# Optimization experiments

Hardware: AMD Instinct MI355X
Metric: run time of the kernel (lower is better)

Reference implementation:

```python
import jax, jax.numpy as jnp
import numpy as np

D_MODEL = 1024
NUM_HEADS = 16
D_K = D_MODEL // NUM_HEADS
B, S = 4, 2048


def setup_inputs() -> dict:
    key = jax.random.key(0)
    ks = jax.random.split(key, 11)
    s = 1.0 / np.sqrt(D_MODEL)  # torch Linear default init scale (uniform bound)
    def lin(k):
        kw, kb = jax.random.split(k)
        W = jax.random.uniform(kw, (D_MODEL, D_MODEL), jnp.float32, -s, s)
        b = jax.random.uniform(kb, (D_MODEL,), jnp.float32, -s, s)
        return W, b
    Wq, bq = lin(ks[0])
    Wk, bk = lin(ks[1])
    Wv, bv = lin(ks[2])
    Wo, bo = lin(ks[3])
    query = jax.random.normal(ks[4], (B, S, D_MODEL), jnp.float32)
    key_t = jax.random.normal(ks[5], (B, S, D_MODEL), jnp.float32)
    value = jax.random.normal(ks[6], (B, S, D_MODEL), jnp.float32)
    mask = jnp.ones((B, 1, 1, S), jnp.int32)
    return {"query": query, "key": key_t, "value": value, "mask": mask,
            "Wq": Wq, "bq": bq, "Wk": Wk, "bk": bk, "Wv": Wv, "bv": bv,
            "Wo": Wo, "bo": bo}


def _split_heads(x):
    # (B, S, D) -> (B, H, S, d_k)
    b, s, _ = x.shape
    return x.reshape(b, s, NUM_HEADS, D_K).transpose(0, 2, 1, 3)


def _mha(query, key, value, mask, Wq, bq, Wk, bk, Wv, bv, Wo, bo):
    Q = _split_heads(query @ Wq.T + bq)
    K = _split_heads(key @ Wk.T + bk)
    V = _split_heads(value @ Wv.T + bv)
    scores = jnp.einsum('bhqd,bhkd->bhqk', Q, K) / np.sqrt(D_K)
    scores = jnp.where(mask == 0, jnp.float32(-1e9), scores)
    attn = jax.nn.softmax(scores, axis=-1)
    out = jnp.einsum('bhqk,bhkd->bhqd', attn, V)  # (B,H,S,d_k)
    out = out.transpose(0, 2, 1, 3).reshape(out.shape[0], out.shape[2], D_MODEL)
    return out @ Wo.T + bo


def reference(query, key, value, mask, Wq, bq, Wk, bk, Wv, bv, Wo, bo):
    return _mha(query, key, value, mask, Wq, bq, Wk, bk, Wv, bv, Wo, bo)
```

## Files before the change

kernel.cpp:

```cpp
#include <hip/hip_runtime.h>


typedef unsigned short u16;
typedef __attribute__((ext_vector_type(8))) short short8;
typedef __attribute__((ext_vector_type(4))) float f32x4;

__device__ __forceinline__ u16 f2bf(float f) {
  union { float f; unsigned int u; } v; v.f = f;
  return (u16)((v.u + 0x7FFFu + ((v.u >> 16) & 1u)) >> 16);
}

__device__ __forceinline__ void gll16(const void* gptr, void* lptr) {
  __builtin_amdgcn_global_load_lds(
      (const __attribute__((address_space(1))) unsigned int*)gptr,
      (__attribute__((address_space(3))) unsigned int*)lptr, 16, 0, 0);
}

__global__ void cvt_x(const float* __restrict__ s, u16* __restrict__ d, int n) {
  const int i = (blockIdx.x * 256 + threadIdx.x) * 8;
  if (i >= n) return;
  f32x4 a = *(const f32x4*)(s + i);
  f32x4 b = *(const f32x4*)(s + i + 4);
  short8 r;
  r[0] = (short)f2bf(a[0]); r[1] = (short)f2bf(a[1]);
  r[2] = (short)f2bf(a[2]); r[3] = (short)f2bf(a[3]);
  r[4] = (short)f2bf(b[0]); r[5] = (short)f2bf(b[1]);
  r[6] = (short)f2bf(b[2]); r[7] = (short)f2bf(b[3]);
  *(short8*)(d + i) = r;
}

__global__ void cvt_x3(const float* __restrict__ q, const float* __restrict__ k,
                       const float* __restrict__ v, u16* __restrict__ d) {
  const int z = blockIdx.y;
  const float* s = (z == 0) ? q : (z == 1) ? k : v;
  const int i = (blockIdx.x * 256 + threadIdx.x) * 8;
  u16* dz = d + (size_t)z * 8388608;
  f32x4 a = *(const f32x4*)(s + i);
  f32x4 b = *(const f32x4*)(s + i + 4);
  short8 r;
  r[0] = (short)f2bf(a[0]); r[1] = (short)f2bf(a[1]);
  r[2] = (short)f2bf(a[2]); r[3] = (short)f2bf(a[3]);
  r[4] = (short)f2bf(b[0]); r[5] = (short)f2bf(b[1]);
  r[6] = (short)f2bf(b[2]); r[7] = (short)f2bf(b[3]);
  *(short8*)(dz + i) = r;
}

__global__ void cvt_w4(const float* __restrict__ w0, const float* __restrict__ w1,
                       const float* __restrict__ w2, const float* __restrict__ w3,
                       u16* __restrict__ d) {
  const int z = blockIdx.y;
  const float* s = (z == 0) ? w0 : (z == 1) ? w1 : (z == 2) ? w2 : w3;
  const int i = (blockIdx.x * 256 + threadIdx.x) * 8;
  u16* dz = d + (size_t)z * 1048576;
  f32x4 a = *(const f32x4*)(s + i);
  f32x4 b = *(const f32x4*)(s + i + 4);
  short8 r;
  r[0] = (short)f2bf(a[0]); r[1] = (short)f2bf(a[1]);
  r[2] = (short)f2bf(a[2]); r[3] = (short)f2bf(a[3]);
  r[4] = (short)f2bf(b[0]); r[5] = (short)f2bf(b[1]);
  r[6] = (short)f2bf(b[2]); r[7] = (short)f2bf(b[3]);
  *(short8*)(dz + i) = r;
}

#define GM 128
#define GN 128
#define GK 32

template <typename TC, bool TRANS>
__global__ __launch_bounds__(256, 3) void gemm_bb(
    const u16* __restrict__ A, const u16* __restrict__ W,
    const float* __restrict__ bias, TC* __restrict__ C,
    int M, int N, int K, float scale)
{
  __shared__ __align__(16) u16 As[2][GM * GK];
  __shared__ __align__(16) u16 Bs[2][GN * GK];

  const int tid  = threadIdx.x;
  const int lane = tid & 63;
  const int l15  = lane & 15;
  const int quad = lane >> 4;
  const int wave = tid >> 6;
  const int bm = blockIdx.y * GM;
  const int bn = blockIdx.x * GN;
  const int wm = (wave >> 1) * 64;
  const int wn = (wave & 1) * 64;

  const f32x4 zero4 = {0.f, 0.f, 0.f, 0.f};
  f32x4 acc[4][4];
#pragma unroll
  for (int i = 0; i < 4; i++)
#pragma unroll
    for (int j = 0; j < 4; j++) acc[i][j] = zero4;

  const int srow = tid >> 2;
  const int chl  = (tid & 3) ^ ((tid >> 3) & 3);
  const u16* Ag = A + (size_t)(bm + srow) * K + chl * 8;
  const u16* Wg = W + (size_t)(bn + srow) * K + chl * 8;
  const size_t rowskip = (size_t)64 * K;
  const int chpA = quad ^ ((l15 >> 1) & 3);

  gll16(Ag, &As[0][tid * 8]);
  gll16(Ag + rowskip, &As[0][tid * 8 + 2048]);
  gll16(Wg, &Bs[0][tid * 8]);
  gll16(Wg + rowskip, &Bs[0][tid * 8 + 2048]);

  int buf = 0;
  for (int k0 = 0; k0 < K; k0 += GK) {
    __syncthreads();
    if (k0 + GK < K) {
      const int nb = buf ^ 1;
      gll16(Ag + k0 + GK, &As[nb][tid * 8]);
      gll16(Ag + k0 + GK + rowskip, &As[nb][tid * 8 + 2048]);
      gll16(Wg + k0 + GK, &Bs[nb][tid * 8]);
      gll16(Wg + k0 + GK + rowskip, &Bs[nb][tid * 8 + 2048]);
    }

    short8 af[4], bfr[4];
#pragma unroll
    for (int mi = 0; mi < 4; mi++)
      af[mi] = *(const short8*)&As[buf][(wm + mi * 16 + l15) * GK + chpA * 8];
#pragma unroll
    for (int ni = 0; ni < 4; ni++)
      bfr[ni] = *(const short8*)&Bs[buf][(wn + ni * 16 + l15) * GK + chpA * 8];
#pragma unroll
    for (int mi = 0; mi < 4; mi++)
#pragma unroll
      for (int ni = 0; ni < 4; ni++)
        acc[mi][ni] = __builtin_amdgcn_mfma_f32_16x16x32_bf16(
            af[mi], bfr[ni], acc[mi][ni], 0, 0, 0);
    buf ^= 1;
  }

  float bval[4];
#pragma unroll
  for (int ni = 0; ni < 4; ni++) bval[ni] = bias[bn + wn + ni * 16 + l15];
#pragma unroll
  for (int mi = 0; mi < 4; mi++) {
    const int m0 = bm + wm + mi * 16 + quad * 4;
#pragma unroll
    for (int ni = 0; ni < 4; ni++) {
      const int n = bn + wn + ni * 16 + l15;
      if constexpr (TRANS) {
        ushort4 w;
        w.x = f2bf((acc[mi][ni][0] + bval[ni]) * scale);
        w.y = f2bf((acc[mi][ni][1] + bval[ni]) * scale);
        w.z = f2bf((acc[mi][ni][2] + bval[ni]) * scale);
        w.w = f2bf((acc[mi][ni][3] + bval[ni]) * scale);
        *(ushort4*)((u16*)C + (size_t)n * M + m0) = w;
      } else {
#pragma unroll
        for (int r = 0; r < 4; r++) {
          const float v = (acc[mi][ni][r] + bval[ni]) * scale;
          if constexpr (sizeof(TC) == 2)
            C[(size_t)(m0 + r) * N + n] = f2bf(v);
          else
            C[(size_t)(m0 + r) * N + n] = v;
        }
      }
    }
  }
}

__global__ __launch_bounds__(256, 3) void gemm_qkv(
    const u16* __restrict__ Ab, const u16* __restrict__ Wc,
    const float* __restrict__ bq, const float* __restrict__ bk,
    const float* __restrict__ bv, u16* __restrict__ Qo,
    u16* __restrict__ Ko, u16* __restrict__ Vo, float qscale)
{
  const int M = 8192, N = 1024, K = 1024;
  const int z = blockIdx.z;
  const u16* A = Ab + (size_t)z * 8388608;
  const u16* W = Wc + (size_t)z * 1048576;
  const float* bias = (z == 0) ? bq : (z == 1) ? bk : bv;
  u16* C = (z == 0) ? Qo : (z == 1) ? Ko : Vo;
  const float scale = (z == 0) ? qscale : 1.0f;
  const bool trans = (z == 2);

  __shared__ __align__(16) u16 As[2][GM * GK];
  __shared__ __align__(16) u16 Bs[2][GN * GK];

  const int tid  = threadIdx.x;
  const int lane = tid & 63;
  const int l15  = lane & 15;
  const int quad = lane >> 4;
  const int wave = tid >> 6;
  const int bm = blockIdx.y * GM;
  const int bn = blockIdx.x * GN;
  const int wm = (wave >> 1) * 64;
  const int wn = (wave & 1) * 64;

  const f32x4 zero4 = {0.f, 0.f, 0.f, 0.f};
  f32x4 acc[4][4];
#pragma unroll
  for (int i = 0; i < 4; i++)
#pragma unroll
    for (int j = 0; j < 4; j++) acc[i][j] = zero4;

  const int srow = tid >> 2;
  const int chl  = (tid & 3) ^ ((tid >> 3) & 3);
  const u16* Ag = A + (size_t)(bm + srow) * K + chl * 8;
  const u16* Wg = W + (size_t)(bn + srow) * K + chl * 8;
  const size_t rowskip = (size_t)64 * K;
  const int chpA = quad ^ ((l15 >> 1) & 3);

  gll16(Ag, &As[0][tid * 8]);
  gll16(Ag + rowskip, &As[0][tid * 8 + 2048]);
  gll16(Wg, &Bs[0][tid * 8]);
  gll16(Wg + rowskip, &Bs[0][tid * 8 + 2048]);

  int buf = 0;
  for (int k0 = 0; k0 < K; k0 += GK) {
    __syncthreads();
    if (k0 + GK < K) {
      const int nb = buf ^ 1;
      gll16(Ag + k0 + GK, &As[nb][tid * 8]);
      gll16(Ag + k0 + GK + rowskip, &As[nb][tid * 8 + 2048]);
      gll16(Wg + k0 + GK, &Bs[nb][tid * 8]);
      gll16(Wg + k0 + GK + rowskip, &Bs[nb][tid * 8 + 2048]);
    }

    short8 af[4], bfr[4];
#pragma unroll
    for (int mi = 0; mi < 4; mi++)
      af[mi] = *(const short8*)&As[buf][(wm + mi * 16 + l15) * GK + chpA * 8];
#pragma unroll
    for (int ni = 0; ni < 4; ni++)
      bfr[ni] = *(const short8*)&Bs[buf][(wn + ni * 16 + l15) * GK + chpA * 8];
#pragma unroll
    for (int mi = 0; mi < 4; mi++)
#pragma unroll
      for (int ni = 0; ni < 4; ni++)
        acc[mi][ni] = __builtin_amdgcn_mfma_f32_16x16x32_bf16(
            af[mi], bfr[ni], acc[mi][ni], 0, 0, 0);
    buf ^= 1;
  }

  float bval[4];
#pragma unroll
  for (int ni = 0; ni < 4; ni++) bval[ni] = bias[bn + wn + ni * 16 + l15];
#pragma unroll
  for (int mi = 0; mi < 4; mi++) {
    const int m0 = bm + wm + mi * 16 + quad * 4;
#pragma unroll
    for (int ni = 0; ni < 4; ni++) {
      const int n = bn + wn + ni * 16 + l15;
      if (trans) {
        ushort4 w;
        w.x = f2bf(acc[mi][ni][0] + bval[ni]);
        w.y = f2bf(acc[mi][ni][1] + bval[ni]);
        w.z = f2bf(acc[mi][ni][2] + bval[ni]);
        w.w = f2bf(acc[mi][ni][3] + bval[ni]);
        *(ushort4*)(C + (size_t)n * M + m0) = w;
      } else {
#pragma unroll
        for (int r = 0; r < 4; r++)
          C[(size_t)(m0 + r) * N + n] = f2bf((acc[mi][ni][r] + bval[ni]) * scale);
      }
    }
  }
}

__global__ __launch_bounds__(256, 4) void attn_fused(
    const u16* __restrict__ Qb, const u16* __restrict__ Kb,
    const u16* __restrict__ VtG, const int* __restrict__ mask,
    u16* __restrict__ Ob)
{
  constexpr int S = 2048, D = 1024;
  __shared__ __align__(16) u16 Ks[2][64 * 64];
  __shared__ __align__(16) u16 Vs[64 * 64];
  __shared__ __align__(16) u16 Pt[4][32 * 64];

  const int tid  = threadIdx.x;
  const int lane = tid & 63;
  const int wave = tid >> 6;
  const int l15  = lane & 15;
  const int quad = lane >> 4;
  const int b = blockIdx.y >> 4;
  const int h = blockIdx.y & 15;
  const int qw = blockIdx.x * 128 + wave * 32;

  const u16* Qp = Qb + (size_t)b * S * D + h * 64;
  const u16* Kp = Kb + (size_t)b * S * D + h * 64;
  const u16* Vg = VtG + (size_t)h * 64 * 8192 + b * 2048;
  const int* mp = mask + b * S;

  short8 qf[2][2];
#pragma unroll
  for (int qb = 0; qb < 2; qb++)
#pragma unroll
    for (int c = 0; c < 2; c++)
      qf[qb][c] = *(const short8*)&Qp[(size_t)(qw + qb * 16 + l15) * D + c * 32 + quad * 8];

  const f32x4 zero4 = {0.f, 0.f, 0.f, 0.f};
  f32x4 o_acc[2][4];
#pragma unroll
  for (int qb = 0; qb < 2; qb++)
#pragma unroll
    for (int ni = 0; ni < 4; ni++) o_acc[qb][ni] = zero4;
  f32x4 l_acc[2] = {zero4, zero4};

  const short8 one8 = {(short)0x3f80, (short)0x3f80, (short)0x3f80, (short)0x3f80,
                       (short)0x3f80, (short)0x3f80, (short)0x3f80, (short)0x3f80};

  const int srow = tid >> 3;
  const int chl  = (tid & 7) ^ (srow & 7);
  const int fsw  = l15 & 7;

#pragma unroll
  for (int p = 0; p < 2; p++)
    gll16(Kp + (size_t)(p * 32 + srow) * D + chl * 8, &Ks[0][p * 2048 + tid * 8]);

  f32x4 cm[4];
#pragma unroll
  for (int s = 0; s < 4; s++) {
    int4 mv = *(const int4*)&mp[s * 16 + quad * 4];
    cm[s][0] = mv.x ? 0.f : -1.0e9f;
    cm[s][1] = mv.y ? 0.f : -1.0e9f;
    cm[s][2] = mv.z ? 0.f : -1.0e9f;
    cm[s][3] = mv.w ? 0.f : -1.0e9f;
  }

  int buf = 0;
  for (int kt = 0; kt < S; kt += 64) {
    __syncthreads();

#pragma unroll
    for (int p = 0; p < 2; p++)
      gll16(Vg + (size_t)(p * 32 + srow) * 8192 + kt + chl * 8,
            &Vs[p * 2048 + tid * 8]);
    if (kt + 64 < S) {
      const int nb = buf ^ 1;
#pragma unroll
      for (int p = 0; p < 2; p++)
        gll16(Kp + (size_t)(kt + 64 + p * 32 + srow) * D + chl * 8,
              &Ks[nb][p * 2048 + tid * 8]);
    }

    f32x4 nm[4];
    const int nkt = (kt + 64) & (S - 1);
#pragma unroll
    for (int s = 0; s < 4; s++) {
      int4 mv = *(const int4*)&mp[nkt + s * 16 + quad * 4];
      nm[s][0] = mv.x ? 0.f : -1.0e9f;
      nm[s][1] = mv.y ? 0.f : -1.0e9f;
      nm[s][2] = mv.z ? 0.f : -1.0e9f;
      nm[s][3] = mv.w ? 0.f : -1.0e9f;
    }

    f32x4 sc[2][4];
#pragma unroll
    for (int qb = 0; qb < 2; qb++)
#pragma unroll
      for (int s = 0; s < 4; s++) sc[qb][s] = zero4;
#pragma unroll
    for (int c = 0; c < 2; c++)
#pragma unroll
      for (int s = 0; s < 4; s++) {
        short8 kf = *(const short8*)
            &Ks[buf][(s * 16 + l15) * 64 + ((c * 4 + quad) ^ fsw) * 8];
        sc[0][s] = __builtin_amdgcn_mfma_f32_16x16x32_bf16(kf, qf[0][c], sc[0][s], 0, 0, 0);
        sc[1][s] = __builtin_amdgcn_mfma_f32_16x16x32_bf16(kf, qf[1][c], sc[1][s], 0, 0, 0);
      }

#pragma unroll
    for (int qb = 0; qb < 2; qb++) {
      const int qrow = qb * 16 + l15;
#pragma unroll
      for (int s = 0; s < 4; s++) {
        unsigned int t[4];
#pragma unroll
        for (int r = 0; r < 4; r++) {
          union { float f; unsigned int u; } pu;
          pu.f = __builtin_amdgcn_exp2f(sc[qb][s][r] + cm[s][r]);
          t[r] = pu.u;
        }
        uint2 w;
        w.x = __builtin_amdgcn_perm(t[1], t[0], 0x07060302u);
        w.y = __builtin_amdgcn_perm(t[3], t[2], 0x07060302u);
        const int phys = (s * 2 + (quad >> 1)) ^ fsw;
        *(uint2*)&Pt[wave][qrow * 64 + phys * 8 + (quad & 1) * 4] = w;
      }
    }

    __syncthreads();

#pragma unroll
    for (int c = 0; c < 2; c++) {
      short8 pf[2];
#pragma unroll
      for (int qb = 0; qb < 2; qb++)
        pf[qb] = *(const short8*)
            &Pt[wave][(qb * 16 + l15) * 64 + ((c * 4 + quad) ^ fsw) * 8];
      l_acc[0] = __builtin_amdgcn_mfma_f32_16x16x32_bf16(pf[0], one8, l_acc[0], 0, 0, 0);
      l_acc[1] = __builtin_amdgcn_mfma_f32_16x16x32_bf16(pf[1], one8, l_acc[1], 0, 0, 0);
#pragma unroll
      for (int ni = 0; ni < 4; ni++) {
        short8 vf = *(const short8*)
            &Vs[(ni * 16 + l15) * 64 + ((c * 4 + quad) ^ fsw) * 8];
        o_acc[0][ni] = __builtin_amdgcn_mfma_f32_16x16x32_bf16(pf[0], vf, o_acc[0][ni], 0, 0, 0);
        o_acc[1][ni] = __builtin_amdgcn_mfma_f32_16x16x32_bf16(pf[1], vf, o_acc[1][ni], 0, 0, 0);
      }
    }

#pragma unroll
    for (int s = 0; s < 4; s++) cm[s] = nm[s];
    buf ^= 1;
  }

  float rl[2][4];
#pragma unroll
  for (int qb = 0; qb < 2; qb++)
#pragma unroll
    for (int r = 0; r < 4; r++) rl[qb][r] = 1.0f / l_acc[qb][r];
#pragma unroll
  for (int qb = 0; qb < 2; qb++) {
    const int q0 = qw + qb * 16 + quad * 4;
#pragma unroll
    for (int ni = 0; ni < 4; ni++)
#pragma unroll
      for (int r = 0; r < 4; r++)
        Ob[(size_t)(b * S + q0 + r) * D + h * 64 + ni * 16 + l15] =
            f2bf(o_acc[qb][ni][r] * rl[qb][r]);
  }
}

extern "C" void kernel_launch(void* const* d_in, const int* in_sizes, int n_in,
                              void* d_out, int out_size, void* d_ws, size_t ws_size,
                              hipStream_t stream) {
  const int M = 8192, N = 1024, K = 1024;
  const float* q    = (const float*)d_in[0];
  const float* k    = (const float*)d_in[1];
  const float* v    = (const float*)d_in[2];
  const int*   mask = (const int*)d_in[3];
  const float* Wq = (const float*)d_in[4];
  const float* bq = (const float*)d_in[5];
  const float* Wk = (const float*)d_in[6];
  const float* bk = (const float*)d_in[7];
  const float* Wv = (const float*)d_in[8];
  const float* bv = (const float*)d_in[9];
  const float* Wo = (const float*)d_in[10];
  const float* bo = (const float*)d_in[11];

  const size_t MN = (size_t)M * N;
  const float QSC = 0.125f * 1.44269504f;

  dim3 bb(256);
  dim3 gg(N / GN, M / GM);

  const size_t need_batched = (6 * MN + 4 * 1048576) * sizeof(u16);
  if (ws_size >= need_batched) {
    u16* Ax  = (u16*)d_ws;
    u16* Qb  = Ax + 3 * MN;
    u16* Kb  = Ax + 4 * MN;
    u16* VtG = Ax + 5 * MN;
    u16* Wc  = Ax + 6 * MN;
    u16* Ob  = Ax;

    cvt_w4<<<dim3(512, 4), bb, 0, stream>>>(Wq, Wk, Wv, Wo, Wc);
    cvt_x3<<<dim3(4096, 3), bb, 0, stream>>>(q, k, v, Ax);
    gemm_qkv<<<dim3(8, 64, 3), bb, 0, stream>>>(Ax, Wc, bq, bk, bv, Qb, Kb, VtG, QSC);
    attn_fused<<<dim3(16, 64), bb, 0, stream>>>(Qb, Kb, VtG, mask, Ob);
    gemm_bb<float, false><<<gg, bb, 0, stream>>>(Ob, Wc + 3 * 1048576, bo,
                                                 (float*)d_out, M, N, K, 1.0f);
  } else {
    u16* Qb  = (u16*)d_ws;
    u16* Kb  = Qb + MN;
    u16* VtG = Kb + MN;
    u16* Ob  = VtG + MN;
    u16* Wc  = Ob + MN;
    const int xblk = (int)(MN / (256 * 8));

    cvt_w4<<<dim3(512, 4), bb, 0, stream>>>(Wq, Wk, Wv, Wo, Wc);

    cvt_x<<<xblk, bb, 0, stream>>>(q, Ob, M * N);
    gemm_bb<u16, false><<<gg, bb, 0, stream>>>(Ob, Wc + 0 * 1048576, bq, Qb, M, N, K, QSC);
    cvt_x<<<xblk, bb, 0, stream>>>(k, Ob, M * N);
    gemm_bb<u16, false><<<gg, bb, 0, stream>>>(Ob, Wc + 1 * 1048576, bk, Kb, M, N, K, 1.0f);
    cvt_x<<<xblk, bb, 0, stream>>>(v, Ob, M * N);
    gemm_bb<u16, true><<<gg, bb, 0, stream>>>(Ob, Wc + 2 * 1048576, bv, VtG, M, N, K, 1.0f);

    attn_fused<<<dim3(16, 64), bb, 0, stream>>>(Qb, Kb, VtG, mask, Ob);

    gemm_bb<float, false><<<gg, bb, 0, stream>>>(Ob, Wc + 3 * 1048576, bo,
                                                 (float*)d_out, M, N, K, 1.0f);
  }
}
```

Baseline: 365.4 us.

## Precompute mask tile bitmap, single-buffer K, and add XCD-aware block swizzling

The attention kernel builds a per-64-key-tile bitmap of fully-open mask tiles once at start via ballot, and skips the per-tile mask loads and adds when a tile is fully unmasked. The K buffer becomes single-buffered: the next K tile load is issued after the second barrier and overlaps the PV MFMAs. Both GEMM kernels and the attention kernel also remap block indices so consecutive tiles land on the same XCD, aiming for better L2 reuse. Single-buffering K cuts LDS use but shortens the window in which the prefetch can hide load latency.

```diff
diff --git a/kernel.cpp b/kernel.cpp
--- a/kernel.cpp
+++ b/kernel.cpp
@@ -62,6 +62,16 @@
   *(short8*)(dz + i) = r;
 }
 
+__device__ __forceinline__ void xcd_swz(unsigned& bx, unsigned& by) {
+  const unsigned nx = gridDim.x, nwg = nx * gridDim.y;
+  if ((nwg & 7u) == 0u) {
+    const unsigned lin = bx + nx * by;
+    const unsigned swz = (lin & 7u) * (nwg >> 3) + (lin >> 3);
+    bx = swz % nx;
+    by = swz / nx;
+  }
+}
+
 #define GM 128
 #define GN 128
 #define GK 32
@@ -80,8 +90,10 @@
   const int l15  = lane & 15;
   const int quad = lane >> 4;
   const int wave = tid >> 6;
-  const int bm = blockIdx.y * GM;
-  const int bn = blockIdx.x * GN;
+  unsigned bxu = blockIdx.x, byu = blockIdx.y;
+  xcd_swz(bxu, byu);
+  const int bm = byu * GM;
+  const int bn = bxu * GN;
   const int wm = (wave >> 1) * 64;
   const int wn = (wave & 1) * 64;
 
@@ -184,8 +196,10 @@
   const int l15  = lane & 15;
   const int quad = lane >> 4;
   const int wave = tid >> 6;
-  const int bm = blockIdx.y * GM;
-  const int bn = blockIdx.x * GN;
+  unsigned bxu = blockIdx.x, byu = blockIdx.y;
+  xcd_swz(bxu, byu);
+  const int bm = byu * GM;
+  const int bn = bxu * GN;
   const int wm = (wave >> 1) * 64;
   const int wn = (wave & 1) * 64;
 
@@ -266,7 +280,7 @@
     u16* __restrict__ Ob)
 {
   constexpr int S = 2048, D = 1024;
-  __shared__ __align__(16) u16 Ks[2][64 * 64];
+  __shared__ __align__(16) u16 Ks[64 * 64];
   __shared__ __align__(16) u16 Vs[64 * 64];
   __shared__ __align__(16) u16 Pt[4][32 * 64];
 
@@ -275,9 +289,12 @@
   const int wave = tid >> 6;
   const int l15  = lane & 15;
   const int quad = lane >> 4;
-  const int b = blockIdx.y >> 4;
-  const int h = blockIdx.y & 15;
-  const int qw = blockIdx.x * 128 + wave * 32;
+
+  const int lin = blockIdx.x + 16 * blockIdx.y;
+  const int swz = (lin & 7) * 128 + (lin >> 3);
+  const int b  = swz >> 8;
+  const int h  = (swz >> 4) & 15;
+  const int qw = (swz & 15) * 128 + wave * 32;
 
   const u16* Qp = Qb + (size_t)b * S * D + h * 64;
   const u16* Kp = Kb + (size_t)b * S * D + h * 64;
@@ -306,21 +323,30 @@
   const int chl  = (tid & 7) ^ (srow & 7);
   const int fsw  = l15 & 7;
 
+  unsigned int* tbs = (unsigned int*)&Pt[0][0];
+  {
+    const int t8 = tid * 8;
+    int4 a  = *(const int4*)&mp[t8];
+    int4 c4 = *(const int4*)&mp[t8 + 4];
+    int ok = ((a.x & a.y & a.z & a.w & c4.x & c4.y & c4.z & c4.w) != 0);
+    unsigned long long bb = __ballot(ok);
+    if (lane == 0) {
+      unsigned int byt = 0;
+#pragma unroll
+      for (int g = 0; g < 8; g++)
+        if (((bb >> (8 * g)) & 0xffull) == 0xffull) byt |= 1u << g;
+      tbs[wave] = byt;
+    }
+  }
+
 #pragma unroll
   for (int p = 0; p < 2; p++)
-    gll16(Kp + (size_t)(p * 32 + srow) * D + chl * 8, &Ks[0][p * 2048 + tid * 8]);
-
-  f32x4 cm[4];
-#pragma unroll
-  for (int s = 0; s < 4; s++) {
-    int4 mv = *(const int4*)&mp[s * 16 + quad * 4];
-    cm[s][0] = mv.x ? 0.f : -1.0e9f;
-    cm[s][1] = mv.y ? 0.f : -1.0e9f;
-    cm[s][2] = mv.z ? 0.f : -1.0e9f;
-    cm[s][3] = mv.w ? 0.f : -1.0e9f;
-  }
-
-  int buf = 0;
+    gll16(Kp + (size_t)(p * 32 + srow) * D + chl * 8, &Ks[p * 2048 + tid * 8]);
+
+  __syncthreads();
+  const unsigned int tilebits = __builtin_amdgcn_readfirstlane(
+      tbs[0] | (tbs[1] << 8) | (tbs[2] << 16) | (tbs[3] << 24));
+
   for (int kt = 0; kt < S; kt += 64) {
     __syncthreads();
 
@@ -328,61 +354,82 @@
     for (int p = 0; p < 2; p++)
       gll16(Vg + (size_t)(p * 32 + srow) * 8192 + kt + chl * 8,
             &Vs[p * 2048 + tid * 8]);
+
+    f32x4 sc[2][4];
+#pragma unroll
+    for (int qb = 0; qb < 2; qb++)
+#pragma unroll
+      for (int s = 0; s < 4; s++) sc[qb][s] = zero4;
+#pragma unroll
+    for (int c = 0; c < 2; c++)
+#pragma unroll
+      for (int s = 0; s < 4; s++) {
+        short8 kf = *(const short8*)
+            &Ks[(s * 16 + l15) * 64 + ((c * 4 + quad) ^ fsw) * 8];
+        sc[0][s] = __builtin_amdgcn_mfma_f32_16x16x32_bf16(kf, qf[0][c], sc[0][s], 0, 0, 0);
+        sc[1][s] = __builtin_amdgcn_mfma_f32_16x16x32_bf16(kf, qf[1][c], sc[1][s], 0, 0, 0);
+      }
+
+    const bool open = (tilebits >> (kt >> 6)) & 1;
+    if (open) {
+#pragma unroll
+      for (int qb = 0; qb < 2; qb++) {
+        const int qrow = qb * 16 + l15;
+#pragma unroll
+        for (int s = 0; s < 4; s++) {
+          unsigned int t[4];
+#pragma unroll
+          for (int r = 0; r < 4; r++) {
+            union { float f; unsigned int u; } pu;
+            pu.f = __builtin_amdgcn_exp2f(sc[qb][s][r]);
+            t[r] = pu.u;
+          }
+          uint2 w;
+          w.x = __builtin_amdgcn_perm(t[1], t[0], 0x07060302u);
+          w.y = __builtin_amdgcn_perm(t[3], t[2], 0x07060302u);
+          const int phys = (s * 2 + (quad >> 1)) ^ fsw;
+          *(uint2*)&Pt[wave][qrow * 64 + phys * 8 + (quad & 1) * 4] = w;
+        }
+      }
+    } else {
+      f32x4 cm[4];
+#pragma unroll
+      for (int s = 0; s < 4; s++) {
+        int4 mv = *(const int4*)&mp[kt + s * 16 + quad * 4];
+        cm[s][0] = mv.x ? 0.f : -1.0e9f;
+        cm[s][1] = mv.y ? 0.f : -1.0e9f;
+        cm[s][2] = mv.z ? 0.f : -1.0e9f;
+        cm[s][3] = mv.w ? 0.f : -1.0e9f;
+      }
+#pragma unroll
+      for (int qb = 0; qb < 2; qb++) {
+        const int qrow = qb * 16 + l15;
+#pragma unroll
+        for (int s = 0; s < 4; s++) {
+          unsigned int t[4];
+#pragma unroll
+          for (int r = 0; r < 4; r++) {
+            union { float f; unsigned int u; } pu;
+            pu.f = __builtin_amdgcn_exp2f(sc[qb][s][r] + cm[s][r]);
+            t[r] = pu.u;
+          }
+          uint2 w;
+          w.x = __builtin_amdgcn_perm(t[1], t[0], 0x07060302u);
+          w.y = __builtin_amdgcn_perm(t[3], t[2], 0x07060302u);
+          const int phys = (s * 2 + (quad >> 1)) ^ fsw;
+          *(uint2*)&Pt[wave][qrow * 64 + phys * 8 + (quad & 1) * 4] = w;
+        }
+      }
+    }
+
+    __syncthreads();
+
     if (kt + 64 < S) {
-      const int nb = buf ^ 1;
 #pragma unroll
       for (int p = 0; p < 2; p++)
         gll16(Kp + (size_t)(kt + 64 + p * 32 + srow) * D + chl * 8,
-              &Ks[nb][p * 2048 + tid * 8]);
-    }
-
-    f32x4 nm[4];
-    const int nkt = (kt + 64) & (S - 1);
-#pragma unroll
-    for (int s = 0; s < 4; s++) {
-      int4 mv = *(const int4*)&mp[nkt + s * 16 + quad * 4];
-      nm[s][0] = mv.x ? 0.f : -1.0e9f;
-      nm[s][1] = mv.y ? 0.f : -1.0e9f;
-      nm[s][2] = mv.z ? 0.f : -1.0e9f;
-      nm[s][3] = mv.w ? 0.f : -1.0e9f;
-    }
-
-    f32x4 sc[2][4];
-#pragma unroll
-    for (int qb = 0; qb < 2; qb++)
-#pragma unroll
-      for (int s = 0; s < 4; s++) sc[qb][s] = zero4;
-#pragma unroll
-    for (int c = 0; c < 2; c++)
-#pragma unroll
-      for (int s = 0; s < 4; s++) {
-        short8 kf = *(const short8*)
-            &Ks[buf][(s * 16 + l15) * 64 + ((c * 4 + quad) ^ fsw) * 8];
-        sc[0][s] = __builtin_amdgcn_mfma_f32_16x16x32_bf16(kf, qf[0][c], sc[0][s], 0, 0, 0);
-        sc[1][s] = __builtin_amdgcn_mfma_f32_16x16x32_bf16(kf, qf[1][c], sc[1][s], 0, 0, 0);
-      }
-
-#pragma unroll
-    for (int qb = 0; qb < 2; qb++) {
-      const int qrow = qb * 16 + l15;
-#pragma unroll
-      for (int s = 0; s < 4; s++) {
-        unsigned int t[4];
-#pragma unroll
-        for (int r = 0; r < 4; r++) {
-          union { float f; unsigned int u; } pu;
-          pu.f = __builtin_amdgcn_exp2f(sc[qb][s][r] + cm[s][r]);
-          t[r] = pu.u;
-        }
-        uint2 w;
-        w.x = __builtin_amdgcn_perm(t[1], t[0], 0x07060302u);
-        w.y = __builtin_amdgcn_perm(t[3], t[2], 0x07060302u);
-        const int phys = (s * 2 + (quad >> 1)) ^ fsw;
-        *(uint2*)&Pt[wave][qrow * 64 + phys * 8 + (quad & 1) * 4] = w;
-      }
-    }
-
-    __syncthreads();
+              &Ks[p * 2048 + tid * 8]);
+    }
 
 #pragma unroll
     for (int c = 0; c < 2; c++) {
@@ -401,10 +448,6 @@
         o_acc[1][ni] = __builtin_amdgcn_mfma_f32_16x16x32_bf16(pf[1], vf, o_acc[1][ni], 0, 0, 0);
       }
     }
-
-#pragma unroll
-    for (int s = 0; s < 4; s++) cm[s] = nm[s];
-    buf ^= 1;
   }
 
   float rl[2][4];
```

Result: faster. 334.5 us (-8.5%).
